# Performance work log

Measured on AMD Instinct MI355X. Metric: run time of the kernel, lower is better.

Reference implementation:

```python
import jax, jax.numpy as jnp
import numpy as np

B, N, L = 256, 128, 2048
NF, AC, HID = 75, 3, 256
DIM, NHEAD, FPD, NWORD = 128, 8, 679, 8600


def setup_inputs() -> dict:
    key = jax.random.key(0)
    ks = iter(jax.random.split(key, 48))
    rn = lambda *s: jax.random.normal(next(ks), s, dtype=jnp.float32) * 0.05
    d = {}
    d['V'] = jax.random.normal(next(ks), (B, N, NF), dtype=jnp.float32)
    d['A'] = jax.random.uniform(next(ks), (B, AC, N, N), dtype=jnp.float32)
    d['fp'] = jax.random.uniform(next(ks), (B, FPD), dtype=jnp.float32)
    d['mol_size'] = jax.random.randint(next(ks), (B,), 1, N + 1, dtype=jnp.int32)
    d['protein_seq'] = jax.random.randint(next(ks), (B, L), 0, NWORD)
    d['label'] = jax.random.randint(next(ks), (B,), 0, 2)
    # GConv blocks (multi-channel GCN): 75->256, 256->256, 256->256
    d['gc_W1'], d['gc_b1'] = rn(AC, NF, HID), rn(HID)
    d['gc_W2'], d['gc_b2'] = rn(AC, HID, HID), rn(HID)
    d['gc_W3'], d['gc_b3'] = rn(AC, HID, HID), rn(HID)
    # fp linear chain: 679->128, 128->128
    d['fp_W1'], d['fp_b1'] = rn(FPD, DIM), rn(DIM)
    d['fp_W2'], d['fp_b2'] = rn(DIM, DIM), rn(DIM)
    # global attention pooling (per-head node scores) + readout
    d['att_W'] = rn(HID, NHEAD)
    d['ro_W'], d['ro_b'] = rn(HID * NHEAD, DIM), rn(DIM)
    d['emb'] = rn(NWORD, DIM)
    # cross-attention projections
    d['mfp_W'], d['mfp_b'] = rn(DIM, DIM), rn(DIM)
    d['pfp_W'], d['pfp_b'] = rn(DIM, DIM), rn(DIM)
    d['mv_W'], d['mv_b'] = rn(DIM, DIM), rn(DIM)
    d['pv_W'], d['pv_b'] = rn(DIM, DIM), rn(DIM)
    # stacked MLPs (3 layers each, width 2*dim)
    d['mlp1_W'], d['mlp1_b'] = rn(3, 2 * DIM, 2 * DIM), rn(3, 2 * DIM)
    d['mlp2_W'], d['mlp2_b'] = rn(3, 2 * DIM, 2 * DIM), rn(3, 2 * DIM)
    d['out1_W'], d['out1_b'] = rn(2 * DIM, 2), rn(2)
    d['out2_W'], d['out2_b'] = rn(2 * DIM, 2), rn(2)
    return d


def _gconv(V, A, W, b):
    # A: [b,c,n,m], V: [b,m,f], W: [c,f,o]
    AV = jnp.einsum('bcnm,bmf->bcnf', A, V)
    return jax.nn.relu(jnp.einsum('bcnf,cfo->bno', AV, W) + b)


def _cross_attn(hvec, prot_emb, mW, mb, pW, pb):
    # hvec: [b,d]; prot_emb: [b,l,d]
    h = jax.nn.relu(hvec @ mW + mb)                       # [b,d]
    hs = jax.nn.relu(jnp.einsum('bld,de->ble', prot_emb, pW) + pb)  # [b,l,d]
    w = jnp.tanh(jnp.einsum('bd,bld->bl', h, hs))         # [b,l]
    ys = w[..., None] * hs                                 # [b,l,d]
    return jnp.max(ys, axis=1)                             # [b,d]


def reference(V, A, fp, mol_size, protein_seq, label,
              gc_W1, gc_b1, gc_W2, gc_b2, gc_W3, gc_b3,
              fp_W1, fp_b1, fp_W2, fp_b2, att_W, ro_W, ro_b, emb,
              mfp_W, mfp_b, pfp_W, pfp_b, mv_W, mv_b, pv_W, pv_b,
              mlp1_W, mlp1_b, mlp2_W, mlp2_b, out1_W, out1_b, out2_W, out2_b):
    # fp linear chain (dropout = identity at inference)
    fp = jax.nn.relu(fp @ fp_W1 + fp_b1)
    fp = jax.nn.relu(fp @ fp_W2 + fp_b2)
    # graph conv blocks
    Vh = _gconv(V, A, gc_W1, gc_b1)
    Vh = _gconv(Vh, A, gc_W2, gc_b2)
    Vh = _gconv(Vh, A, gc_W3, gc_b3)
    # masked multi-head global attention pooling over nodes
    scores = jnp.einsum('bnf,fh->bnh', Vh, att_W)          # [b,n,heads]
    mask = jnp.arange(N)[None, :] < mol_size[:, None]       # [b,n]
    scores = jnp.where(mask[..., None], scores, -1e9)
    att = jax.nn.softmax(scores, axis=1)
    pooled = jnp.einsum('bnh,bnf->bhf', att, Vh).reshape(Vh.shape[0], -1)  # [b, heads*nf]
    Vr = jax.nn.relu(pooled @ ro_W + ro_b)                  # [b,dim]
    # protein embedding + ragged cross-attention branches
    prot_emb = emb[protein_seq]                             # [b,l,dim]
    itact1 = _cross_attn(fp, prot_emb, mfp_W, mfp_b, pfp_W, pfp_b)
    itact2 = _cross_attn(Vr, prot_emb, mv_W, mv_b, pv_W, pv_b)
    cat1 = jnp.concatenate([fp, itact1], axis=1)
    cat2 = jnp.concatenate([Vr, itact2], axis=1)
    for i in range(mlp1_W.shape[0]):
        cat1 = jax.nn.relu(cat1 @ mlp1_W[i] + mlp1_b[i])
        cat2 = jax.nn.relu(cat2 @ mlp2_W[i] + mlp2_b[i])
    pred_itact = (cat1 @ out1_W + out1_b) + (cat2 @ out2_W + out2_b)
    pred_labels = jnp.argmax(pred_itact, axis=1)
    pred_scores = jax.nn.softmax(pred_itact, axis=1)[:, 1]
    return (pred_itact, label, pred_labels, pred_scores)
```

## Files before the change

### kernel.cpp

```cpp
#include <hip/hip_runtime.h>
#include <math.h>

static constexpr int BB   = 256;
static constexpr int NN   = 128;
static constexpr int LL   = 2048;
static constexpr int NF   = 75;
static constexpr int AC   = 3;
static constexpr int HID  = 256;
static constexpr int DIM  = 128;
static constexpr int NHEAD= 8;
static constexpr int FPD  = 679;
static constexpr int FPDP = 704;
static constexpr int NWORD= 8600;
static constexpr int NWP  = 8704;
static constexpr int KB   = 768;

typedef __attribute__((ext_vector_type(8))) _Float16 f16x8;
typedef __attribute__((ext_vector_type(4))) float f32x4;
typedef unsigned int u32;
typedef unsigned short u16;

__device__ __forceinline__ u16 f2h(float x) {
    _Float16 h = (_Float16)x;
    return *(u16*)&h;
}
__device__ __forceinline__ u16 f2h_sat(float x) {
    x = fminf(fmaxf(x, -65000.f), 65000.f);
    _Float16 h = (_Float16)x;
    return *(u16*)&h;
}
__device__ __forceinline__ float h2f(u16 x) {
    return (float)(*(_Float16*)&x);
}

static constexpr float SC   = 0.0625f;
static constexpr float USC  = 16.0f;

__global__ __launch_bounds__(256)
void prepA_kernel(const float* __restrict__ A, u16* __restrict__ Ah)
{
    size_t base = (size_t)blockIdx.x * (NN * NN);
    int t = threadIdx.x;
    #pragma unroll
    for (int i = 0; i < 16; ++i) {
        int id = t + i * 256;
        float4 v = *(const float4*)(A + base + (size_t)id * 4);
        u32 p0 = (u32)f2h(v.x) | ((u32)f2h(v.y) << 16);
        u32 p1 = (u32)f2h(v.z) | ((u32)f2h(v.w) << 16);
        *(uint2*)(Ah + base + (size_t)id * 4) = make_uint2(p0, p1);
    }
}

__global__ __launch_bounds__(256)
void prepFp_kernel(const float* __restrict__ fp, u16* __restrict__ fph)
{
    int b = blockIdx.x, t = threadIdx.x;
    for (int i = t; i < FPDP; i += 256) {
        float v = (i < FPD) ? fp[(size_t)b * FPD + i] : 0.f;
        fph[(size_t)b * FPDP + i] = f2h(v);
    }
}

__global__ __launch_bounds__(256)
void prepFpW_kernel(const float* __restrict__ fpW1, const float* __restrict__ fpW2,
                    u16* __restrict__ W1t, u16* __restrict__ W2t)
{
    int o = blockIdx.x, z = blockIdx.y, t = threadIdx.x;
    if (z == 0) {
        for (int k = t; k < FPDP; k += 256) {
            float v = (k < FPD) ? fpW1[(size_t)k * DIM + o] : 0.f;
            W1t[(size_t)o * FPDP + k] = f2h(v);
        }
    } else {
        if (t < 128) W2t[(size_t)o * 128 + t] = f2h(fpW2[(size_t)t * DIM + o]);
    }
}

__global__ __launch_bounds__(128)
void prepCrossW_kernel(const float* __restrict__ pfpW, const float* __restrict__ pvW,
                       const float* __restrict__ mfpW, const float* __restrict__ mvW,
                       u16* __restrict__ pWt12, u16* __restrict__ mWt12)
{
    int o = blockIdx.x, z = blockIdx.y, t = threadIdx.x;
    const float* W = (z == 0) ? pfpW : (z == 1) ? pvW : (z == 2) ? mfpW : mvW;
    u16* Wt = (z < 2) ? (pWt12 + (size_t)z * 128 * 128)
                      : (mWt12 + (size_t)(z - 2) * 128 * 128);
    Wt[(size_t)o * 128 + t] = f2h(W[(size_t)t * 128 + o]);
}

__global__ __launch_bounds__(256)
void prepMlpW_kernel(const float* __restrict__ m1W, const float* __restrict__ m2W,
                     u16* __restrict__ Wmlp)
{
    int o = blockIdx.x, Lr = blockIdx.y, br = blockIdx.z, t = threadIdx.x;
    const float* W = (br ? m2W : m1W) + (size_t)Lr * 256 * 256;
    Wmlp[(((size_t)(br * 3 + Lr)) * 256 + o) * 256 + t] = f2h(W[(size_t)t * 256 + o]);
}

__global__ __launch_bounds__(256)
void fp1_mfma(const u16* __restrict__ fph, const u16* __restrict__ W1t,
              const float* __restrict__ b1, u16* __restrict__ FP1h)
{
    __shared__ u16 As[128 * 40];
    __shared__ u16 Bs[128 * 40];
    int mt = blockIdx.x;
    const u16* Ap = fph + (size_t)(mt * 128) * FPDP;

    int t = threadIdx.x;
    int l = t & 63, wid = t >> 6;
    int rb = (wid >> 1) * 64, cb = (wid & 1) * 64;
    int ln = l & 15, q = l >> 4;

    f32x4 acc[4][4] = {};

    for (int kt = 0; kt < FPDP / 32; ++kt) {
        #pragma unroll
        for (int i = 0; i < 2; ++i) {
            int id = t + i * 256;
            int row = id >> 2, qh = id & 3;
            *(uint4*)&As[row * 40 + qh * 8] =
                *(const uint4*)(Ap + (size_t)row * FPDP + kt * 32 + qh * 8);
            *(uint4*)&Bs[row * 40 + qh * 8] =
                *(const uint4*)(W1t + (size_t)row * FPDP + kt * 32 + qh * 8);
        }
        __syncthreads();
        f16x8 af[4], bfr[4];
        #pragma unroll
        for (int fr = 0; fr < 4; ++fr)
            af[fr] = *(const f16x8*)&As[(rb + fr * 16 + ln) * 40 + q * 8];
        #pragma unroll
        for (int fc = 0; fc < 4; ++fc)
            bfr[fc] = *(const f16x8*)&Bs[(cb + fc * 16 + ln) * 40 + q * 8];
        #pragma unroll
        for (int fr = 0; fr < 4; ++fr)
            #pragma unroll
            for (int fc = 0; fc < 4; ++fc)
                acc[fr][fc] = __builtin_amdgcn_mfma_f32_16x16x32_f16(
                    af[fr], bfr[fc], acc[fr][fc], 0, 0, 0);
        __syncthreads();
    }
    #pragma unroll
    for (int fr = 0; fr < 4; ++fr)
        #pragma unroll
        for (int fc = 0; fc < 4; ++fc) {
            int d = cb + fc * 16 + ln;
            float bv = b1[d];
            #pragma unroll
            for (int r = 0; r < 4; ++r) {
                int m = rb + fr * 16 + q * 4 + r;
                FP1h[(size_t)(mt * 128 + m) * 128 + d] = f2h(fmaxf(acc[fr][fc][r] + bv, 0.f));
            }
        }
}

__global__ __launch_bounds__(256)
void fp2_mfma(const u16* __restrict__ FP1h, const u16* __restrict__ W2t,
              const float* __restrict__ b2, float* __restrict__ FP2,
              u16* __restrict__ FP2h)
{
    __shared__ u16 As[128 * 40];
    __shared__ u16 Bs[128 * 40];
    int mt = blockIdx.x;
    const u16* Ap = FP1h + (size_t)(mt * 128) * 128;

    int t = threadIdx.x;
    int l = t & 63, wid = t >> 6;
    int rb = (wid >> 1) * 64, cb = (wid & 1) * 64;
    int ln = l & 15, q = l >> 4;

    f32x4 acc[4][4] = {};

    for (int kt = 0; kt < 4; ++kt) {
        #pragma unroll
        for (int i = 0; i < 2; ++i) {
            int id = t + i * 256;
            int row = id >> 2, qh = id & 3;
            *(uint4*)&As[row * 40 + qh * 8] =
                *(const uint4*)(Ap + (size_t)row * 128 + kt * 32 + qh * 8);
            *(uint4*)&Bs[row * 40 + qh * 8] =
                *(const uint4*)(W2t + (size_t)row * 128 + kt * 32 + qh * 8);
        }
        __syncthreads();
        f16x8 af[4], bfr[4];
        #pragma unroll
        for (int fr = 0; fr < 4; ++fr)
            af[fr] = *(const f16x8*)&As[(rb + fr * 16 + ln) * 40 + q * 8];
        #pragma unroll
        for (int fc = 0; fc < 4; ++fc)
            bfr[fc] = *(const f16x8*)&Bs[(cb + fc * 16 + ln) * 40 + q * 8];
        #pragma unroll
        for (int fr = 0; fr < 4; ++fr)
            #pragma unroll
            for (int fc = 0; fc < 4; ++fc)
                acc[fr][fc] = __builtin_amdgcn_mfma_f32_16x16x32_f16(
                    af[fr], bfr[fc], acc[fr][fc], 0, 0, 0);
        __syncthreads();
    }
    #pragma unroll
    for (int fr = 0; fr < 4; ++fr)
        #pragma unroll
        for (int fc = 0; fc < 4; ++fc) {
            int d = cb + fc * 16 + ln;
            float bv = b2[d];
            #pragma unroll
            for (int r = 0; r < 4; ++r) {
                int m = rb + fr * 16 + q * 4 + r;
                float val = fmaxf(acc[fr][fc][r] + bv, 0.f);
                FP2 [(size_t)(mt * 128 + m) * 128 + d] = val;
                FP2h[(size_t)(mt * 128 + m) * 128 + d] = f2h(val);
            }
        }
}

__global__ __launch_bounds__(256)
void hs12_mfma(const float* __restrict__ emb, const u16* __restrict__ pWt12,
               const float* __restrict__ ba, const float* __restrict__ bb_,
               u16* __restrict__ HS12)
{
    __shared__ u16 As[128 * 40];
    __shared__ u16 Bs[128 * 40];
    int ft = blockIdx.x, br = blockIdx.y;
    const u16* Bp = pWt12 + (size_t)br * 128 * 128;
    const float* bias = br ? bb_ : ba;
    int r0 = ft * 128;

    int t = threadIdx.x;
    int l = t & 63, wid = t >> 6;
    int rb = (wid >> 1) * 64, cb = (wid & 1) * 64;
    int ln = l & 15, q = l >> 4;

    f32x4 acc[4][4] = {};

    for (int kt = 0; kt < 4; ++kt) {
        #pragma unroll
        for (int i = 0; i < 4; ++i) {
            int id = t + i * 256;
            int row = id >> 3, qf = id & 7;
            int r = r0 + row;
            float4 v = make_float4(0.f, 0.f, 0.f, 0.f);
            if (r < NWORD) v = *(const float4*)(emb + (size_t)r * 128 + kt * 32 + qf * 4);
            u32 p0 = (u32)f2h(v.x) | ((u32)f2h(v.y) << 16);
            u32 p1 = (u32)f2h(v.z) | ((u32)f2h(v.w) << 16);
            u32* dst = (u32*)&As[row * 40 + qf * 4];
            dst[0] = p0; dst[1] = p1;
        }
        #pragma unroll
        for (int i = 0; i < 2; ++i) {
            int id = t + i * 256;
            int row = id >> 2, qh = id & 3;
            *(uint4*)&Bs[row * 40 + qh * 8] =
                *(const uint4*)(Bp + (size_t)row * 128 + kt * 32 + qh * 8);
        }
        __syncthreads();
        f16x8 af[4], bfr[4];
        #pragma unroll
        for (int fr = 0; fr < 4; ++fr)
            af[fr] = *(const f16x8*)&As[(rb + fr * 16 + ln) * 40 + q * 8];
        #pragma unroll
        for (int fc = 0; fc < 4; ++fc)
            bfr[fc] = *(const f16x8*)&Bs[(cb + fc * 16 + ln) * 40 + q * 8];
        #pragma unroll
        for (int fr = 0; fr < 4; ++fr)
            #pragma unroll
            for (int fc = 0; fc < 4; ++fc)
                acc[fr][fc] = __builtin_amdgcn_mfma_f32_16x16x32_f16(
                    af[fr], bfr[fc], acc[fr][fc], 0, 0, 0);
        __syncthreads();
    }
    #pragma unroll
    for (int fr = 0; fr < 4; ++fr)
        #pragma unroll
        for (int fc = 0; fc < 4; ++fc) {
            int d = cb + fc * 16 + ln;
            float bv = bias[d];
            #pragma unroll
            for (int r = 0; r < 4; ++r) {
                int m = rb + fr * 16 + q * 4 + r;
                int rr = r0 + m;
                if (rr < NWORD)
                    HS12[(size_t)rr * 256 + br * 128 + d] = f2h(fmaxf(acc[fr][fc][r] + bv, 0.f));
            }
        }
}

__global__ __launch_bounds__(256)
void prepVt_kernel(const float* __restrict__ V, u16* __restrict__ Vt)
{
    int b = blockIdx.x, t = threadIdx.x;
    __shared__ float sV[NN * NF];
    for (int i = t; i < NN * NF; i += 256) sV[i] = V[(size_t)b * (NN * NF) + i];
    __syncthreads();
    for (int i = t; i < 80 * 128; i += 256) {
        int f = i >> 7, n = i & 127;
        float v = (f < NF) ? sV[n * NF + f] : 0.f;
        Vt[(size_t)b * (80 * 128) + i] = f2h(v);
    }
}

__global__ __launch_bounds__(256)
void prepW_kernel(const float* __restrict__ W1, const float* __restrict__ W2,
                  const float* __restrict__ W3, u16* __restrict__ Wt1,
                  u16* __restrict__ Wt2, u16* __restrict__ Wt3)
{
    int o = blockIdx.x, z = blockIdx.y, t = threadIdx.x;
    if (z == 0) {
        int k = t;
        int c = k / 80, f = k - c * 80;
        float v = (c < 3 && f < NF) ? W1[((size_t)c * NF + f) * HID + o] : 0.f;
        Wt1[(size_t)o * 256 + k] = f2h(v);
    } else {
        const float* W = (z == 1) ? W2 : W3;
        u16* Wt = (z == 1) ? Wt2 : Wt3;
        for (int k = t; k < KB; k += 256) {
            int c = k >> 8, f = k & 255;
            Wt[(size_t)o * KB + k] = f2h(W[((size_t)c * HID + f) * HID + o]);
        }
    }
}

__global__ __launch_bounds__(256)
void gA_mfma(const u16* __restrict__ Agr, const u16* __restrict__ Htr,
             u16* __restrict__ AV, int b0, int htStride, int fpMul, int Fvalid)
{
    __shared__ u16 As[128 * 40];
    __shared__ u16 Bs[128 * 40];
    int ft = blockIdx.x, c = blockIdx.y, bl = blockIdx.z;
    int b = b0 + bl;
    const u16* Ap = Agr + ((size_t)b * AC + c) * (NN * NN);
    const u16* Bp = Htr + (size_t)b * htStride + ft * (128 * 128);
    u16* Cp = AV + (size_t)bl * (NN * KB) + c * fpMul + ft * 128;

    int t = threadIdx.x;
    int l = t & 63, wid = t >> 6;
    int rb = (wid >> 1) * 64, cb = (wid & 1) * 64;
    int ln = l & 15, q = l >> 4;

    f32x4 acc[4][4] = {};

    for (int kt = 0; kt < 4; ++kt) {
        #pragma unroll
        for (int i = 0; i < 2; ++i) {
            int id = t + i * 256;
            int row = id >> 2, qh = id & 3;
            *(uint4*)&As[row * 40 + qh * 8] =
                *(const uint4*)(Ap + (size_t)row * NN + kt * 32 + qh * 8);
        }
        #pragma unroll
        for (int i = 0; i < 2; ++i) {
            int id = t + i * 256;
            int row = id >> 2, qh = id & 3;
            uint4 v = make_uint4(0, 0, 0, 0);
            if (row < Fvalid) v = *(const uint4*)(Bp + (size_t)row * 128 + kt * 32 + qh * 8);
            *(uint4*)&Bs[row * 40 + qh * 8] = v;
        }
        __syncthreads();
        f16x8 af[4], bfr[4];
        #pragma unroll
        for (int fr = 0; fr < 4; ++fr)
            af[fr] = *(const f16x8*)&As[(rb + fr * 16 + ln) * 40 + q * 8];
        #pragma unroll
        for (int fc = 0; fc < 4; ++fc)
            bfr[fc] = *(const f16x8*)&Bs[(cb + fc * 16 + ln) * 40 + q * 8];
        #pragma unroll
        for (int fr = 0; fr < 4; ++fr)
            #pragma unroll
            for (int fc = 0; fc < 4; ++fc)
                acc[fr][fc] = __builtin_amdgcn_mfma_f32_16x16x32_f16(
                    af[fr], bfr[fc], acc[fr][fc], 0, 0, 0);
        __syncthreads();
    }
    #pragma unroll
    for (int fr = 0; fr < 4; ++fr) {
        #pragma unroll
        for (int fc = 0; fc < 4; ++fc) {
            int fcol = cb + fc * 16 + ln;
            if (fcol < Fvalid) {
                #pragma unroll
                for (int r = 0; r < 4; ++r) {
                    int n = rb + fr * 16 + q * 4 + r;
                    Cp[(size_t)n * KB + fcol] = f2h_sat(acc[fr][fc][r] * SC);
                }
            }
        }
    }
}

__global__ __launch_bounds__(256)
void gB_mfma(const u16* __restrict__ AV, const u16* __restrict__ Wt,
             const float* __restrict__ bias, u16* __restrict__ Hout,
             int b0, int kTiles, int Ks, int mode)
{
    __shared__ u16 As[128 * 40];
    __shared__ u16 Bs[128 * 40];
    __shared__ u16 sLT[128][136];
    int ot = blockIdx.x, bl = blockIdx.y;
    int b = b0 + bl;
    const u16* Ap = AV + (size_t)bl * (NN * KB);
    const u16* Bp = Wt + (size_t)ot * 128 * Ks;

    int t = threadIdx.x;
    int l = t & 63, wid = t >> 6;
    int rb = (wid >> 1) * 64, cb = (wid & 1) * 64;
    int ln = l & 15, q = l >> 4;

    f32x4 acc[4][4] = {};

    for (int kt = 0; kt < kTiles; ++kt) {
        #pragma unroll
        for (int i = 0; i < 2; ++i) {
            int id = t + i * 256;
            int row = id >> 2, qh = id & 3;
            *(uint4*)&As[row * 40 + qh * 8] =
                *(const uint4*)(Ap + (size_t)row * KB + kt * 32 + qh * 8);
            *(uint4*)&Bs[row * 40 + qh * 8] =
                *(const uint4*)(Bp + (size_t)row * Ks + kt * 32 + qh * 8);
        }
        __syncthreads();
        f16x8 af[4], bfr[4];
        #pragma unroll
        for (int fr = 0; fr < 4; ++fr)
            af[fr] = *(const f16x8*)&As[(rb + fr * 16 + ln) * 40 + q * 8];
        #pragma unroll
        for (int fc = 0; fc < 4; ++fc)
            bfr[fc] = *(const f16x8*)&Bs[(cb + fc * 16 + ln) * 40 + q * 8];
        #pragma unroll
        for (int fr = 0; fr < 4; ++fr)
            #pragma unroll
            for (int fc = 0; fc < 4; ++fc)
                acc[fr][fc] = __builtin_amdgcn_mfma_f32_16x16x32_f16(
                    af[fr], bfr[fc], acc[fr][fc], 0, 0, 0);
        __syncthreads();
    }
    if (mode == 0) {
        #pragma unroll
        for (int fr = 0; fr < 4; ++fr)
            #pragma unroll
            for (int fc = 0; fc < 4; ++fc) {
                int oc = cb + fc * 16 + ln;
                float bv = bias[ot * 128 + oc];
                #pragma unroll
                for (int r = 0; r < 4; ++r) {
                    int n = rb + fr * 16 + q * 4 + r;
                    sLT[oc][n] = f2h_sat(fmaxf(acc[fr][fc][r] * USC + bv, 0.f));
                }
            }
        __syncthreads();
        int row = t >> 1, half = t & 1;
        u16* dst = Hout + ((size_t)b * HID + ot * 128 + row) * NN + half * 64;
        #pragma unroll
        for (int j = 0; j < 8; ++j)
            *(uint4*)(dst + j * 8) = *(const uint4*)&sLT[row][half * 64 + j * 8];
    } else {
        #pragma unroll
        for (int fr = 0; fr < 4; ++fr)
            #pragma unroll
            for (int fc = 0; fc < 4; ++fc) {
                int oc = cb + fc * 16 + ln;
                float bv = bias[ot * 128 + oc];
                #pragma unroll
                for (int r = 0; r < 4; ++r) {
                    int n = rb + fr * 16 + q * 4 + r;
                    float val = fmaxf(acc[fr][fc][r] * USC + bv, 0.f);
                    Hout[((size_t)b * NN + n) * HID + ot * 128 + oc] = f2h_sat(val * SC);
                }
            }
    }
}

__global__ __launch_bounds__(256)
void pool_kernel(const u16* __restrict__ H3h,
                 const float* __restrict__ attW,
                 const int* __restrict__ msz,
                 float* __restrict__ pooled)
{
    int b = blockIdx.x, t = threadIdx.x;
    __shared__ u16  sTh[128][264];
    __shared__ float sW[HID * NHEAD];
    __shared__ float sS[NN * NHEAD];
    __shared__ float sP[16][NHEAD][2];
    for (int i = t; i < HID * NHEAD; i += 256) sW[i] = attW[i];
    const u16* Hb = H3h + (size_t)b * NN * HID;
    for (int i = t; i < 128 * 32; i += 256) {
        int row = i >> 5, fq = (i & 31) * 8;
        *(uint4*)&sTh[row][fq] = *(const uint4*)(Hb + (size_t)row * HID + fq);
    }
    __syncthreads();
    for (int n0 = 0; n0 < NN; n0 += 16) {
        int nl = t >> 4, h = (t >> 1) & 7, fh = t & 1;
        float s = 0.f;
        for (int f = fh * 128; f < fh * 128 + 128; ++f)
            s += h2f(sTh[n0 + nl][f]) * sW[f * NHEAD + h];
        sP[nl][h][fh] = s;
        __syncthreads();
        if (t < 128) {
            int n2 = t >> 3, h2 = t & 7;
            sS[(n0 + n2) * NHEAD + h2] = USC * (sP[n2][h2][0] + sP[n2][h2][1]);
        }
        __syncthreads();
    }
    int ms = msz[b];
    int h = t >> 5, ln = t & 31;
    float mx = -1e9f;
    for (int n = ln; n < NN; n += 32) {
        float s = (n < ms) ? sS[n * NHEAD + h] : -1e9f;
        mx = fmaxf(mx, s);
    }
    #pragma unroll
    for (int off = 16; off; off >>= 1) mx = fmaxf(mx, __shfl_xor(mx, off, 32));
    float sum = 0.f;
    for (int n = ln; n < NN; n += 32) {
        float s = (n < ms) ? sS[n * NHEAD + h] : -1e9f;
        sum += expf(s - mx);
    }
    #pragma unroll
    for (int off = 16; off; off >>= 1) sum += __shfl_xor(sum, off, 32);
    float inv = 1.f / sum;
    for (int n = ln; n < NN; n += 32) {
        float s = (n < ms) ? sS[n * NHEAD + h] : -1e9f;
        sS[n * NHEAD + h] = expf(s - mx) * inv;
    }
    __syncthreads();
    float accp[NHEAD] = {};
    for (int n = 0; n < NN; ++n) {
        float hv = h2f(sTh[n][t]);
        #pragma unroll
        for (int hh = 0; hh < NHEAD; ++hh) accp[hh] += sS[n * NHEAD + hh] * hv;
    }
    #pragma unroll
    for (int hh = 0; hh < NHEAD; ++hh)
        pooled[(size_t)b * (HID * NHEAD) + hh * HID + t] = USC * accp[hh];
}

__global__ __launch_bounds__(128)
void readout_part(const float* __restrict__ pooled,
                  const float* __restrict__ roW,
                  float* __restrict__ Rp)
{
    int b = blockIdx.x, s = blockIdx.y, t = threadIdx.x;
    __shared__ float sx[256];
    const float* sp = pooled + (size_t)b * (HID * NHEAD) + s * 256;
    sx[t] = sp[t];
    sx[t + 128] = sp[t + 128];
    __syncthreads();
    float acc = 0.f;
    const float* W = roW + (size_t)(s * 256) * DIM + t;
    for (int k = 0; k < 256; ++k) acc += sx[k] * W[(size_t)k * DIM];
    Rp[((size_t)s * BB + b) * DIM + t] = acc;
}

__global__ __launch_bounds__(128)
void readout_merge(const float* __restrict__ Rp,
                   const float* __restrict__ rob,
                   float* __restrict__ Vr, u16* __restrict__ Vrh)
{
    int b = blockIdx.x, t = threadIdx.x;
    float a = rob[t];
    #pragma unroll
    for (int s = 0; s < 8; ++s) a += Rp[((size_t)s * BB + b) * DIM + t];
    float v = fmaxf(a, 0.f);
    Vr [(size_t)b * DIM + t] = v;
    Vrh[(size_t)b * DIM + t] = f2h_sat(v * SC);
}

__global__ __launch_bounds__(256)
void atth_mfma(const u16* __restrict__ FP2h, const u16* __restrict__ VRh,
               const u16* __restrict__ mWt12,
               const float* __restrict__ mfpb, const float* __restrict__ mvb,
               float* __restrict__ h1v, float* __restrict__ h2v)
{
    __shared__ u16 As[128 * 40];
    __shared__ u16 Bs[128 * 40];
    int mt = blockIdx.x, br = blockIdx.y;
    const u16* Ap = (br ? VRh : FP2h) + (size_t)(mt * 128) * 128;
    const u16* Bp = mWt12 + (size_t)br * 128 * 128;
    const float* bias = br ? mvb : mfpb;
    float unsc = br ? USC : 1.f;
    float* out = br ? h2v : h1v;

    int t = threadIdx.x;
    int l = t & 63, wid = t >> 6;
    int rb = (wid >> 1) * 64, cb = (wid & 1) * 64;
    int ln = l & 15, q = l >> 4;

    f32x4 acc[4][4] = {};

    for (int kt = 0; kt < 4; ++kt) {
        #pragma unroll
        for (int i = 0; i < 2; ++i) {
            int id = t + i * 256;
            int row = id >> 2, qh = id & 3;
            *(uint4*)&As[row * 40 + qh * 8] =
                *(const uint4*)(Ap + (size_t)row * 128 + kt * 32 + qh * 8);
            *(uint4*)&Bs[row * 40 + qh * 8] =
                *(const uint4*)(Bp + (size_t)row * 128 + kt * 32 + qh * 8);
        }
        __syncthreads();
        f16x8 af[4], bfr[4];
        #pragma unroll
        for (int fr = 0; fr < 4; ++fr)
            af[fr] = *(const f16x8*)&As[(rb + fr * 16 + ln) * 40 + q * 8];
        #pragma unroll
        for (int fc = 0; fc < 4; ++fc)
            bfr[fc] = *(const f16x8*)&Bs[(cb + fc * 16 + ln) * 40 + q * 8];
        #pragma unroll
        for (int fr = 0; fr < 4; ++fr)
            #pragma unroll
            for (int fc = 0; fc < 4; ++fc)
                acc[fr][fc] = __builtin_amdgcn_mfma_f32_16x16x32_f16(
                    af[fr], bfr[fc], acc[fr][fc], 0, 0, 0);
        __syncthreads();
    }
    #pragma unroll
    for (int fr = 0; fr < 4; ++fr)
        #pragma unroll
        for (int fc = 0; fc < 4; ++fc) {
            int d = cb + fc * 16 + ln;
            float bv = bias[d];
            #pragma unroll
            for (int r = 0; r < 4; ++r) {
                int m = rb + fr * 16 + q * 4 + r;
                out[(size_t)(mt * 128 + m) * 128 + d] = fmaxf(acc[fr][fc][r] * unsc + bv, 0.f);
            }
        }
}

__global__ __launch_bounds__(256)
void cross_part_kernel(const int* __restrict__ seq,
                       const u16* __restrict__ HS12,
                       const float* __restrict__ h1v, const float* __restrict__ h2v,
                       float* __restrict__ Pc)
{
    int b = blockIdx.x, s = blockIdx.y, t = threadIdx.x;
    int g = t >> 4, gl = t & 15;
    int d0 = gl * 8;
    float h1[8], h2[8];
    #pragma unroll
    for (int j = 0; j < 8; ++j) {
        h1[j] = h1v[(size_t)b * DIM + d0 + j];
        h2[j] = h2v[(size_t)b * DIM + d0 + j];
    }
    float m1[8], m2[8];
    #pragma unroll
    for (int j = 0; j < 8; ++j) { m1[j] = -INFINITY; m2[j] = -INFINITY; }
    const int* sq = seq + (size_t)b * LL + s * 256;
    for (int it = 0; it < 16; ++it) {
        int tok = sq[g + 16 * it];
        const u16* r12 = HS12 + (size_t)tok * 256 + d0;
        f16x8 va16 = *(const f16x8*)(r12);
        f16x8 vb16 = *(const f16x8*)(r12 + 128);
        float va[8], vb[8];
        float p1 = 0.f, p2 = 0.f;
        #pragma unroll
        for (int j = 0; j < 8; ++j) {
            va[j] = (float)va16[j];
            vb[j] = (float)vb16[j];
            p1 += h1[j] * va[j];
            p2 += h2[j] * vb[j];
        }
        #pragma unroll
        for (int off = 8; off; off >>= 1) {
            p1 += __shfl_xor(p1, off);
            p2 += __shfl_xor(p2, off);
        }
        float w1 = tanhf(p1), w2 = tanhf(p2);
        #pragma unroll
        for (int j = 0; j < 8; ++j) {
            m1[j] = fmaxf(m1[j], w1 * va[j]);
            m2[j] = fmaxf(m2[j], w2 * vb[j]);
        }
    }
    __shared__ float red[16][2][DIM];
    #pragma unroll
    for (int j = 0; j < 8; ++j) { red[g][0][d0 + j] = m1[j]; red[g][1][d0 + j] = m2[j]; }
    __syncthreads();
    int tb = t >> 7, d = t & 127;
    float mx = red[0][tb][d];
    #pragma unroll
    for (int gg = 1; gg < 16; ++gg) mx = fmaxf(mx, red[gg][tb][d]);
    Pc[(((size_t)s * BB + b) * 2 + tb) * DIM + d] = mx;
}

__global__ __launch_bounds__(256)
void cross_merge_kernel(const float* __restrict__ Pc,
                        float* __restrict__ IT1, float* __restrict__ IT2)
{
    int b = blockIdx.x, t = threadIdx.x;
    float m = -INFINITY;
    for (int s = 0; s < 8; ++s)
        m = fmaxf(m, Pc[((size_t)s * BB + b) * 256 + t]);
    if (t < DIM) IT1[(size_t)b * DIM + t] = m;
    else         IT2[(size_t)b * DIM + t - DIM] = m;
}

__global__ __launch_bounds__(256)
void prepX_kernel(const float* __restrict__ FP2, const float* __restrict__ VR,
                  const float* __restrict__ IT1, const float* __restrict__ IT2,
                  u16* __restrict__ Xh)
{
    int b = blockIdx.x, br = blockIdx.y, t = threadIdx.x;
    const float* a0 = br ? VR : FP2;
    const float* a1 = br ? IT2 : IT1;
    float v = (t < 128) ? a0[(size_t)b * 128 + t] : a1[(size_t)b * 128 + t - 128];
    Xh[((size_t)br * BB + b) * 256 + t] = f2h_sat(v * SC);
}

__global__ __launch_bounds__(256)
void mlpL_mfma(const u16* __restrict__ X, const u16* __restrict__ Wmlp,
               const float* __restrict__ m1b, const float* __restrict__ m2b,
               int Lr, u16* __restrict__ Y)
{
    __shared__ u16 As[128 * 40];
    __shared__ u16 Bs[128 * 40];
    int mt = blockIdx.x, ot = blockIdx.y, br = blockIdx.z;
    const u16* Ap = X + ((size_t)br * BB + mt * 128) * 256;
    const u16* Bp = Wmlp + (((size_t)(br * 3 + Lr)) * 256 + ot * 128) * 256;
    const float* bias = (br ? m2b : m1b) + (size_t)Lr * 256 + ot * 128;

    int t = threadIdx.x;
    int l = t & 63, wid = t >> 6;
    int rb = (wid >> 1) * 64, cb = (wid & 1) * 64;
    int ln = l & 15, q = l >> 4;

    f32x4 acc[4][4] = {};

    for (int kt = 0; kt < 8; ++kt) {
        #pragma unroll
        for (int i = 0; i < 2; ++i) {
            int id = t + i * 256;
            int row = id >> 2, qh = id & 3;
            *(uint4*)&As[row * 40 + qh * 8] =
                *(const uint4*)(Ap + (size_t)row * 256 + kt * 32 + qh * 8);
            *(uint4*)&Bs[row * 40 + qh * 8] =
                *(const uint4*)(Bp + (size_t)row * 256 + kt * 32 + qh * 8);
        }
        __syncthreads();
        f16x8 af[4], bfr[4];
        #pragma unroll
        for (int fr = 0; fr < 4; ++fr)
            af[fr] = *(const f16x8*)&As[(rb + fr * 16 + ln) * 40 + q * 8];
        #pragma unroll
        for (int fc = 0; fc < 4; ++fc)
            bfr[fc] = *(const f16x8*)&Bs[(cb + fc * 16 + ln) * 40 + q * 8];
        #pragma unroll
        for (int fr = 0; fr < 4; ++fr)
            #pragma unroll
            for (int fc = 0; fc < 4; ++fc)
                acc[fr][fc] = __builtin_amdgcn_mfma_f32_16x16x32_f16(
                    af[fr], bfr[fc], acc[fr][fc], 0, 0, 0);
        __syncthreads();
    }
    #pragma unroll
    for (int fr = 0; fr < 4; ++fr)
        #pragma unroll
        for (int fc = 0; fc < 4; ++fc) {
            int oc = cb + fc * 16 + ln;
            float bv = bias[oc] * SC;
            #pragma unroll
            for (int r = 0; r < 4; ++r) {
                int m = rb + fr * 16 + q * 4 + r;
                Y[((size_t)br * BB + (mt * 128 + m)) * 256 + ot * 128 + oc] =
                    f2h_sat(fmaxf(acc[fr][fc][r] + bv, 0.f));
            }
        }
}

__global__ __launch_bounds__(256)
void mlp_out_kernel(const u16* __restrict__ Y,
                    const float* __restrict__ o1W, const float* __restrict__ o1b,
                    const float* __restrict__ o2W, const float* __restrict__ o2b,
                    const int* __restrict__ label,
                    float* __restrict__ dout)
{
    int b = blockIdx.x, t = threadIdx.x;
    __shared__ float pl[2][128];
    const u16* y1 = Y + (size_t)b * 256;
    const u16* y2 = Y + ((size_t)BB + b) * 256;
    int j = t & 1, k2 = t >> 1;
    float p = USC * (h2f(y1[k2])       * o1W[k2 * 2 + j]
                   + h2f(y1[k2 + 128]) * o1W[(k2 + 128) * 2 + j]
                   + h2f(y2[k2])       * o2W[k2 * 2 + j]
                   + h2f(y2[k2 + 128]) * o2W[(k2 + 128) * 2 + j]);
    pl[j][k2] = p;
    __syncthreads();
    for (int s = 64; s > 0; s >>= 1) {
        if (k2 < s) pl[j][k2] += pl[j][k2 + s];
        __syncthreads();
    }
    if (t == 0) {
        float l0 = pl[0][0] + o1b[0] + o2b[0];
        float l1 = pl[1][0] + o1b[1] + o2b[1];
        dout[(size_t)b * 2 + 0] = l0;
        dout[(size_t)b * 2 + 1] = l1;
        dout[2 * BB + b] = (float)label[b];
        dout[3 * BB + b] = (float)((l1 > l0) ? 1 : 0);
        float mx = fmaxf(l0, l1);
        float e0 = expf(l0 - mx), e1 = expf(l1 - mx);
        dout[4 * BB + b] = e1 / (e0 + e1);
    }
}

extern "C" void kernel_launch(void* const* d_in, const int* in_sizes, int n_in,
                              void* d_out, int out_size, void* d_ws, size_t ws_size,
                              hipStream_t stream)
{
    const float* V    = (const float*)d_in[0];
    const float* A    = (const float*)d_in[1];
    const float* fp   = (const float*)d_in[2];
    const int*   msz  = (const int*)  d_in[3];
    const int*   seq  = (const int*)  d_in[4];
    const int*   lab  = (const int*)  d_in[5];
    const float* gcW1 = (const float*)d_in[6];  const float* gcb1 = (const float*)d_in[7];
    const float* gcW2 = (const float*)d_in[8];  const float* gcb2 = (const float*)d_in[9];
    const float* gcW3 = (const float*)d_in[10]; const float* gcb3 = (const float*)d_in[11];
    const float* fpW1 = (const float*)d_in[12]; const float* fpb1 = (const float*)d_in[13];
    const float* fpW2 = (const float*)d_in[14]; const float* fpb2 = (const float*)d_in[15];
    const float* attW = (const float*)d_in[16];
    const float* roW  = (const float*)d_in[17]; const float* rob  = (const float*)d_in[18];
    const float* emb  = (const float*)d_in[19];
    const float* mfpW = (const float*)d_in[20]; const float* mfpb = (const float*)d_in[21];
    const float* pfpW = (const float*)d_in[22]; const float* pfpb = (const float*)d_in[23];
    const float* mvW  = (const float*)d_in[24]; const float* mvb  = (const float*)d_in[25];
    const float* pvW  = (const float*)d_in[26]; const float* pvb  = (const float*)d_in[27];
    const float* m1W  = (const float*)d_in[28]; const float* m1b  = (const float*)d_in[29];
    const float* m2W  = (const float*)d_in[30]; const float* m2b  = (const float*)d_in[31];
    const float* o1W  = (const float*)d_in[32]; const float* o1b  = (const float*)d_in[33];
    const float* o2W  = (const float*)d_in[34]; const float* o2b  = (const float*)d_in[35];
    float* dout = (float*)d_out;

    char* ws = (char*)d_ws;
    size_t off = 0;
    auto alloc = [&](size_t bytes) -> char* {
        char* p = ws + off;
        off += (bytes + 255) & ~(size_t)255;
        return p;
    };
    u16*   Ah    = (u16*)  alloc((size_t)BB * AC * NN * NN * 2);
    u16*   Vt    = (u16*)  alloc((size_t)BB * 80 * 128 * 2);
    u16*   Wt1   = (u16*)  alloc((size_t)256 * 256 * 2);
    u16*   Wt2   = (u16*)  alloc((size_t)256 * KB * 2);
    u16*   Wt3   = (u16*)  alloc((size_t)256 * KB * 2);
    u16*   Ht    = (u16*)  alloc((size_t)BB * HID * NN * 2);
    u16*   H3h   = (u16*)  alloc((size_t)BB * NN * HID * 2);
    u16*   fph   = (u16*)  alloc((size_t)BB * FPDP * 2);
    u16*   W1t   = (u16*)  alloc((size_t)DIM * FPDP * 2);
    u16*   W2t   = (u16*)  alloc((size_t)DIM * DIM * 2);
    u16*   FP1h  = (u16*)  alloc((size_t)BB * DIM * 2);
    float* FP2   = (float*)alloc((size_t)BB * DIM * 4);
    u16*   FP2h  = (u16*)  alloc((size_t)BB * DIM * 2);
    u16*   pWt12 = (u16*)  alloc((size_t)2 * 128 * 128 * 2);
    u16*   mWt12 = (u16*)  alloc((size_t)2 * 128 * 128 * 2);
    u16*   HS12  = (u16*)  alloc((size_t)NWP * 256 * 2);
    float* PO    = (float*)alloc((size_t)BB * HID * NHEAD * 4);
    float* VR    = (float*)alloc((size_t)BB * DIM * 4);
    u16*   VRh   = (u16*)  alloc((size_t)BB * DIM * 2);
    float* H1V   = (float*)alloc((size_t)BB * DIM * 4);
    float* H2V   = (float*)alloc((size_t)BB * DIM * 4);
    float* IT1   = (float*)alloc((size_t)BB * DIM * 4);
    float* IT2   = (float*)alloc((size_t)BB * DIM * 4);
    float* Pc    = (float*)alloc((size_t)8 * BB * 2 * DIM * 4);
    float* Rp    = (float*)alloc((size_t)8 * BB * DIM * 4);
    u16*   Wmlp  = (u16*)  alloc((size_t)2 * 3 * 256 * 256 * 2);
    u16*   Xa    = (u16*)  alloc((size_t)2 * BB * 256 * 2);
    u16*   Xb    = (u16*)  alloc((size_t)2 * BB * 256 * 2);
    size_t fixedBytes = off;

    int CB = 8;
    size_t perB = (size_t)NN * KB * 2;
    {
        const int tiers[] = {256, 128, 64, 32, 16, 8, 4, 2, 1};
        for (int i = 0; i < 9; ++i)
            if (fixedBytes + (size_t)tiers[i] * perB <= ws_size) { CB = tiers[i]; break; }
    }
    u16* AV = (u16*)(ws + fixedBytes);

    prepA_kernel<<<BB * AC, 256, 0, stream>>>(A, Ah);
    prepVt_kernel<<<BB, 256, 0, stream>>>(V, Vt);
    prepW_kernel<<<dim3(256, 3), 256, 0, stream>>>(gcW1, gcW2, gcW3, Wt1, Wt2, Wt3);
    prepFp_kernel<<<BB, 256, 0, stream>>>(fp, fph);
    prepFpW_kernel<<<dim3(128, 2), 256, 0, stream>>>(fpW1, fpW2, W1t, W2t);
    prepCrossW_kernel<<<dim3(128, 4), 128, 0, stream>>>(pfpW, pvW, mfpW, mvW, pWt12, mWt12);
    prepMlpW_kernel<<<dim3(256, 3, 2), 256, 0, stream>>>(m1W, m2W, Wmlp);
    fp1_mfma<<<2, 256, 0, stream>>>(fph, W1t, fpb1, FP1h);
    fp2_mfma<<<2, 256, 0, stream>>>(FP1h, W2t, fpb2, FP2, FP2h);
    hs12_mfma<<<dim3(NWP / 128, 2), 256, 0, stream>>>(emb, pWt12, pfpb, pvb, HS12);

    for (int b0 = 0; b0 < BB; b0 += CB) {
        gA_mfma<<<dim3(1, AC, CB), 256, 0, stream>>>(Ah, Vt, AV, b0, 80 * 128, 80, 80);
        gB_mfma<<<dim3(2, CB), 256, 0, stream>>>(AV, Wt1, gcb1, Ht, b0, 8, 256, 0);
    }
    for (int b0 = 0; b0 < BB; b0 += CB) {
        gA_mfma<<<dim3(2, AC, CB), 256, 0, stream>>>(Ah, Ht, AV, b0, HID * NN, 256, 128);
        gB_mfma<<<dim3(2, CB), 256, 0, stream>>>(AV, Wt2, gcb2, Ht, b0, 24, KB, 0);
    }
    for (int b0 = 0; b0 < BB; b0 += CB) {
        gA_mfma<<<dim3(2, AC, CB), 256, 0, stream>>>(Ah, Ht, AV, b0, HID * NN, 256, 128);
        gB_mfma<<<dim3(2, CB), 256, 0, stream>>>(AV, Wt3, gcb3, H3h, b0, 24, KB, 1);
    }

    pool_kernel<<<BB, 256, 0, stream>>>(H3h, attW, msz, PO);
    readout_part<<<dim3(BB, 8), 128, 0, stream>>>(PO, roW, Rp);
    readout_merge<<<BB, 128, 0, stream>>>(Rp, rob, VR, VRh);
    atth_mfma<<<dim3(2, 2), 256, 0, stream>>>(FP2h, VRh, mWt12, mfpb, mvb, H1V, H2V);
    cross_part_kernel<<<dim3(BB, 8), 256, 0, stream>>>(seq, HS12, H1V, H2V, Pc);
    cross_merge_kernel<<<BB, 256, 0, stream>>>(Pc, IT1, IT2);
    prepX_kernel<<<dim3(BB, 2), 256, 0, stream>>>(FP2, VR, IT1, IT2, Xa);
    mlpL_mfma<<<dim3(2, 2, 2), 256, 0, stream>>>(Xa, Wmlp, m1b, m2b, 0, Xb);
    mlpL_mfma<<<dim3(2, 2, 2), 256, 0, stream>>>(Xb, Wmlp, m1b, m2b, 1, Xa);
    mlpL_mfma<<<dim3(2, 2, 2), 256, 0, stream>>>(Xa, Wmlp, m1b, m2b, 2, Xb);
    mlp_out_kernel<<<BB, 256, 0, stream>>>(Xb, o1W, o1b, o2W, o2b, lab, dout);
}
```

Baseline: 507.6 us.

## Add A-reusing gconv kernel, fp16 packed cross-attention, fuse cross merge into prepX

Adds a gA2 kernel that loads the per-channel adjacency tile into shared memory once and loops over both feature tiles. This replaces two blocks that each reloaded A. The cross-attention partial kernel now uses fp16 query vectors with packed fdot2 dot products, a fast exp-based tanh, and packed half-precision multiply/max. The cross_merge kernel is folded into prepX to remove one launch and the intermediate buffers. In exchange, the gconv grid has fewer blocks, and the reduced precision in the attention max could change results slightly.

```diff
diff --git a/kernel.cpp b/kernel.cpp
--- a/kernel.cpp
+++ b/kernel.cpp
@@ -16,6 +16,7 @@
 static constexpr int KB   = 768;
 
 typedef __attribute__((ext_vector_type(8))) _Float16 f16x8;
+typedef __attribute__((ext_vector_type(2))) _Float16 h2v;
 typedef __attribute__((ext_vector_type(4))) float f32x4;
 typedef unsigned int u32;
 typedef unsigned short u16;
@@ -386,6 +387,72 @@
 }
 
 __global__ __launch_bounds__(256)
+void gA2_mfma(const u16* __restrict__ Agr, const u16* __restrict__ Htr,
+              u16* __restrict__ AV, int b0)
+{
+    __shared__ u16 As[4][128 * 40];
+    __shared__ u16 Bs[128 * 40];
+    int c = blockIdx.x, bl = blockIdx.y;
+    int b = b0 + bl;
+    const u16* Ap = Agr + ((size_t)b * AC + c) * (NN * NN);
+    u16* Cp0 = AV + (size_t)bl * (NN * KB) + c * 256;
+
+    int t = threadIdx.x;
+    int l = t & 63, wid = t >> 6;
+    int rb = (wid >> 1) * 64, cb = (wid & 1) * 64;
+    int ln = l & 15, q = l >> 4;
+
+    #pragma unroll
+    for (int i = 0; i < 8; ++i) {
+        int id = t + i * 256;
+        int row = id >> 4, kq = id & 15;
+        int kt = kq >> 2, qh = kq & 3;
+        *(uint4*)&As[kt][row * 40 + qh * 8] =
+            *(const uint4*)(Ap + (size_t)row * NN + kt * 32 + qh * 8);
+    }
+
+    for (int ft = 0; ft < 2; ++ft) {
+        const u16* Bp = Htr + (size_t)b * (HID * NN) + ft * (128 * 128);
+        f32x4 acc[4][4] = {};
+        for (int kt = 0; kt < 4; ++kt) {
+            __syncthreads();
+            #pragma unroll
+            for (int i = 0; i < 2; ++i) {
+                int id = t + i * 256;
+                int row = id >> 2, qh = id & 3;
+                *(uint4*)&Bs[row * 40 + qh * 8] =
+                    *(const uint4*)(Bp + (size_t)row * 128 + kt * 32 + qh * 8);
+            }
+            __syncthreads();
+            f16x8 af[4], bfr[4];
+            #pragma unroll
+            for (int fr = 0; fr < 4; ++fr)
+                af[fr] = *(const f16x8*)&As[kt][(rb + fr * 16 + ln) * 40 + q * 8];
+            #pragma unroll
+            for (int fc = 0; fc < 4; ++fc)
+                bfr[fc] = *(const f16x8*)&Bs[(cb + fc * 16 + ln) * 40 + q * 8];
+            #pragma unroll
+            for (int fr = 0; fr < 4; ++fr)
+                #pragma unroll
+                for (int fc = 0; fc < 4; ++fc)
+                    acc[fr][fc] = __builtin_amdgcn_mfma_f32_16x16x32_f16(
+                        af[fr], bfr[fc], acc[fr][fc], 0, 0, 0);
+        }
+        #pragma unroll
+        for (int fr = 0; fr < 4; ++fr)
+            #pragma unroll
+            for (int fc = 0; fc < 4; ++fc) {
+                int fcol = ft * 128 + cb + fc * 16 + ln;
+                #pragma unroll
+                for (int r = 0; r < 4; ++r) {
+                    int n = rb + fr * 16 + q * 4 + r;
+                    Cp0[(size_t)n * KB + fcol] = f2h_sat(acc[fr][fc][r] * SC);
+                }
+            }
+    }
+}
+
+__global__ __launch_bounds__(256)
 void gB_mfma(const u16* __restrict__ AV, const u16* __restrict__ Wt,
              const float* __restrict__ bias, u16* __restrict__ Hout,
              int b0, int kTiles, int Ks, int mode)
@@ -566,7 +633,7 @@
 void atth_mfma(const u16* __restrict__ FP2h, const u16* __restrict__ VRh,
                const u16* __restrict__ mWt12,
                const float* __restrict__ mfpb, const float* __restrict__ mvb,
-               float* __restrict__ h1v, float* __restrict__ h2v)
+               u16* __restrict__ h1h, u16* __restrict__ h2h)
 {
     __shared__ u16 As[128 * 40];
     __shared__ u16 Bs[128 * 40];
@@ -575,7 +642,7 @@
     const u16* Bp = mWt12 + (size_t)br * 128 * 128;
     const float* bias = br ? mvb : mfpb;
     float unsc = br ? USC : 1.f;
-    float* out = br ? h2v : h1v;
+    u16* out = br ? h2h : h1h;
 
     int t = threadIdx.x;
     int l = t & 63, wid = t >> 6;
@@ -619,7 +686,8 @@
             #pragma unroll
             for (int r = 0; r < 4; ++r) {
                 int m = rb + fr * 16 + q * 4 + r;
-                out[(size_t)(mt * 128 + m) * 128 + d] = fmaxf(acc[fr][fc][r] * unsc + bv, 0.f);
+                out[(size_t)(mt * 128 + m) * 128 + d] =
+                    f2h_sat(fmaxf(acc[fr][fc][r] * unsc + bv, 0.f));
             }
         }
 }
@@ -627,51 +695,61 @@
 __global__ __launch_bounds__(256)
 void cross_part_kernel(const int* __restrict__ seq,
                        const u16* __restrict__ HS12,
-                       const float* __restrict__ h1v, const float* __restrict__ h2v,
+                       const u16* __restrict__ h1h, const u16* __restrict__ h2h,
                        float* __restrict__ Pc)
 {
     int b = blockIdx.x, s = blockIdx.y, t = threadIdx.x;
     int g = t >> 4, gl = t & 15;
     int d0 = gl * 8;
-    float h1[8], h2[8];
-    #pragma unroll
-    for (int j = 0; j < 8; ++j) {
-        h1[j] = h1v[(size_t)b * DIM + d0 + j];
-        h2[j] = h2v[(size_t)b * DIM + d0 + j];
-    }
-    float m1[8], m2[8];
-    #pragma unroll
-    for (int j = 0; j < 8; ++j) { m1[j] = -INFINITY; m2[j] = -INFINITY; }
+    f16x8 h1 = *(const f16x8*)(h1h + (size_t)b * DIM + d0);
+    f16x8 h2 = *(const f16x8*)(h2h + (size_t)b * DIM + d0);
+    const h2v* h1p = (const h2v*)&h1;
+    const h2v* h2p = (const h2v*)&h2;
+    h2v m1[4], m2[4];
+    _Float16 NEGBIG = (_Float16)(-65504.f);
+    #pragma unroll
+    for (int k = 0; k < 4; ++k) { m1[k] = (h2v){NEGBIG, NEGBIG}; m2[k] = (h2v){NEGBIG, NEGBIG}; }
     const int* sq = seq + (size_t)b * LL + s * 256;
     for (int it = 0; it < 16; ++it) {
         int tok = sq[g + 16 * it];
         const u16* r12 = HS12 + (size_t)tok * 256 + d0;
-        f16x8 va16 = *(const f16x8*)(r12);
-        f16x8 vb16 = *(const f16x8*)(r12 + 128);
-        float va[8], vb[8];
+        f16x8 va = *(const f16x8*)(r12);
+        f16x8 vb = *(const f16x8*)(r12 + 128);
+        const h2v* vap = (const h2v*)&va;
+        const h2v* vbp = (const h2v*)&vb;
         float p1 = 0.f, p2 = 0.f;
         #pragma unroll
-        for (int j = 0; j < 8; ++j) {
-            va[j] = (float)va16[j];
-            vb[j] = (float)vb16[j];
-            p1 += h1[j] * va[j];
-            p2 += h2[j] * vb[j];
+        for (int k = 0; k < 4; ++k) {
+            p1 = __builtin_amdgcn_fdot2(vap[k], h1p[k], p1, false);
+            p2 = __builtin_amdgcn_fdot2(vbp[k], h2p[k], p2, false);
         }
         #pragma unroll
         for (int off = 8; off; off >>= 1) {
             p1 += __shfl_xor(p1, off);
             p2 += __shfl_xor(p2, off);
         }
-        float w1 = tanhf(p1), w2 = tanhf(p2);
-        #pragma unroll
-        for (int j = 0; j < 8; ++j) {
-            m1[j] = fmaxf(m1[j], w1 * va[j]);
-            m2[j] = fmaxf(m2[j], w2 * vb[j]);
+        float w1 = 1.f - 2.f / (__expf(2.f * p1) + 1.f);
+        float w2 = 1.f - 2.f / (__expf(2.f * p2) + 1.f);
+        _Float16 w1s = (_Float16)w1, w2s = (_Float16)w2;
+        h2v w1p = (h2v){w1s, w1s}, w2p = (h2v){w2s, w2s};
+        #pragma unroll
+        for (int k = 0; k < 4; ++k) {
+            h2v pr1 = w1p * vap[k];
+            h2v pr2 = w2p * vbp[k];
+            m1[k] = (h2v){ m1[k][0] > pr1[0] ? m1[k][0] : pr1[0],
+                           m1[k][1] > pr1[1] ? m1[k][1] : pr1[1] };
+            m2[k] = (h2v){ m2[k][0] > pr2[0] ? m2[k][0] : pr2[0],
+                           m2[k][1] > pr2[1] ? m2[k][1] : pr2[1] };
         }
     }
     __shared__ float red[16][2][DIM];
     #pragma unroll
-    for (int j = 0; j < 8; ++j) { red[g][0][d0 + j] = m1[j]; red[g][1][d0 + j] = m2[j]; }
+    for (int k = 0; k < 4; ++k) {
+        red[g][0][d0 + 2 * k]     = (float)m1[k][0];
+        red[g][0][d0 + 2 * k + 1] = (float)m1[k][1];
+        red[g][1][d0 + 2 * k]     = (float)m2[k][0];
+        red[g][1][d0 + 2 * k + 1] = (float)m2[k][1];
+    }
     __syncthreads();
     int tb = t >> 7, d = t & 127;
     float mx = red[0][tb][d];
@@ -681,26 +759,21 @@
 }
 
 __global__ __launch_bounds__(256)
-void cross_merge_kernel(const float* __restrict__ Pc,
-                        float* __restrict__ IT1, float* __restrict__ IT2)
-{
-    int b = blockIdx.x, t = threadIdx.x;
-    float m = -INFINITY;
-    for (int s = 0; s < 8; ++s)
-        m = fmaxf(m, Pc[((size_t)s * BB + b) * 256 + t]);
-    if (t < DIM) IT1[(size_t)b * DIM + t] = m;
-    else         IT2[(size_t)b * DIM + t - DIM] = m;
-}
-
-__global__ __launch_bounds__(256)
 void prepX_kernel(const float* __restrict__ FP2, const float* __restrict__ VR,
-                  const float* __restrict__ IT1, const float* __restrict__ IT2,
-                  u16* __restrict__ Xh)
+                  const float* __restrict__ Pc, u16* __restrict__ Xh)
 {
     int b = blockIdx.x, br = blockIdx.y, t = threadIdx.x;
-    const float* a0 = br ? VR : FP2;
-    const float* a1 = br ? IT2 : IT1;
-    float v = (t < 128) ? a0[(size_t)b * 128 + t] : a1[(size_t)b * 128 + t - 128];
+    float v;
+    if (t < 128) {
+        v = (br ? VR : FP2)[(size_t)b * 128 + t];
+    } else {
+        int d = t - 128;
+        float m = -INFINITY;
+        #pragma unroll
+        for (int s = 0; s < 8; ++s)
+            m = fmaxf(m, Pc[(((size_t)s * BB + b) * 2 + br) * DIM + d]);
+        v = m;
+    }
     Xh[((size_t)br * BB + b) * 256 + t] = f2h_sat(v * SC);
 }
 
@@ -853,10 +926,8 @@
     float* PO    = (float*)alloc((size_t)BB * HID * NHEAD * 4);
     float* VR    = (float*)alloc((size_t)BB * DIM * 4);
     u16*   VRh   = (u16*)  alloc((size_t)BB * DIM * 2);
-    float* H1V   = (float*)alloc((size_t)BB * DIM * 4);
-    float* H2V   = (float*)alloc((size_t)BB * DIM * 4);
-    float* IT1   = (float*)alloc((size_t)BB * DIM * 4);
-    float* IT2   = (float*)alloc((size_t)BB * DIM * 4);
+    u16*   h1h   = (u16*)  alloc((size_t)BB * DIM * 2);
+    u16*   h2h   = (u16*)  alloc((size_t)BB * DIM * 2);
     float* Pc    = (float*)alloc((size_t)8 * BB * 2 * DIM * 4);
     float* Rp    = (float*)alloc((size_t)8 * BB * DIM * 4);
     u16*   Wmlp  = (u16*)  alloc((size_t)2 * 3 * 256 * 256 * 2);
@@ -889,21 +960,20 @@
         gB_mfma<<<dim3(2, CB), 256, 0, stream>>>(AV, Wt1, gcb1, Ht, b0, 8, 256, 0);
     }
     for (int b0 = 0; b0 < BB; b0 += CB) {
-        gA_mfma<<<dim3(2, AC, CB), 256, 0, stream>>>(Ah, Ht, AV, b0, HID * NN, 256, 128);
+        gA2_mfma<<<dim3(AC, CB), 256, 0, stream>>>(Ah, Ht, AV, b0);
         gB_mfma<<<dim3(2, CB), 256, 0, stream>>>(AV, Wt2, gcb2, Ht, b0, 24, KB, 0);
     }
     for (int b0 = 0; b0 < BB; b0 += CB) {
-        gA_mfma<<<dim3(2, AC, CB), 256, 0, stream>>>(Ah, Ht, AV, b0, HID * NN, 256, 128);
+        gA2_mfma<<<dim3(AC, CB), 256, 0, stream>>>(Ah, Ht, AV, b0);
         gB_mfma<<<dim3(2, CB), 256, 0, stream>>>(AV, Wt3, gcb3, H3h, b0, 24, KB, 1);
     }
 
     pool_kernel<<<BB, 256, 0, stream>>>(H3h, attW, msz, PO);
     readout_part<<<dim3(BB, 8), 128, 0, stream>>>(PO, roW, Rp);
     readout_merge<<<BB, 128, 0, stream>>>(Rp, rob, VR, VRh);
-    atth_mfma<<<dim3(2, 2), 256, 0, stream>>>(FP2h, VRh, mWt12, mfpb, mvb, H1V, H2V);
-    cross_part_kernel<<<dim3(BB, 8), 256, 0, stream>>>(seq, HS12, H1V, H2V, Pc);
-    cross_merge_kernel<<<BB, 256, 0, stream>>>(Pc, IT1, IT2);
-    prepX_kernel<<<dim3(BB, 2), 256, 0, stream>>>(FP2, VR, IT1, IT2, Xa);
+    atth_mfma<<<dim3(2, 2), 256, 0, stream>>>(FP2h, VRh, mWt12, mfpb, mvb, h1h, h2h);
+    cross_part_kernel<<<dim3(BB, 8), 256, 0, stream>>>(seq, HS12, h1h, h2h, Pc);
+    prepX_kernel<<<dim3(BB, 2), 256, 0, stream>>>(FP2, VR, Pc, Xa);
     mlpL_mfma<<<dim3(2, 2, 2), 256, 0, stream>>>(Xa, Wmlp, m1b, m2b, 0, Xb);
     mlpL_mfma<<<dim3(2, 2, 2), 256, 0, stream>>>(Xb, Wmlp, m1b, m2b, 1, Xa);
     mlpL_mfma<<<dim3(2, 2, 2), 256, 0, stream>>>(Xa, Wmlp, m1b, m2b, 2, Xb);
```

Result: faster. 494.8 us (-2.5%).
